# Kernel optimization log

Measured on AMD Instinct MI355X. Metric: run time of the kernel, lower is better.

## Reference

```python
import jax, jax.numpy as jnp
import numpy as np

V_K = 1.0
SIGMA = 0.1
EPS = 1e-10


def setup_inputs() -> dict:
    key = jax.random.key(0)
    ks = jax.random.split(key, 5)
    M, L, N, d, H = 2, 6, 512, 2, 64
    data = jax.random.normal(ks[0], (M, L, N, d), dtype=jnp.float32)
    t_snapshots = jnp.arange(L, dtype=jnp.float32) * 0.1
    w1 = jax.random.normal(ks[1], (H,), dtype=jnp.float32) * 0.5
    b1 = jnp.zeros((H,), jnp.float32)
    W2 = jax.random.normal(ks[2], (H, H), dtype=jnp.float32) / np.float32(np.sqrt(H))
    b2 = jnp.zeros((H,), jnp.float32)
    w3 = jax.random.normal(ks[3], (H,), dtype=jnp.float32) / np.float32(np.sqrt(H))
    b3 = jnp.zeros((), jnp.float32)
    return {"data": data, "t_snapshots": t_snapshots, "w1": w1, "b1": b1,
            "W2": W2, "b2": b2, "w3": w3, "b3": b3}


def _phi(r, w1, b1, W2, b2, w3, b3):
    # scalar-to-scalar tanh MLP applied elementwise to r (any shape)
    h1 = jnp.tanh(r[..., None] * w1 + b1)                      # [..., H]
    h2 = jnp.tanh(jnp.einsum('...h,hk->...k', h1, W2) + b2)    # [..., H]
    return jnp.einsum('...k,k->...', h2, w3) + b3              # [...]


def _loss(data, t, params):
    M, L, N, d = data.shape
    diff = data[:, :, :, None, :] - data[:, :, None, :, :]     # [M,L,N,N,d]
    ssq = jnp.sum(diff * diff, axis=-1)                        # [M,L,N,N]
    dist = jnp.where(ssq > 0, jnp.sqrt(jnp.where(ssq > 0, ssq, 1.0)), 0.0)
    off_diag = ~jnp.eye(N, dtype=bool)                         # [N,N]

    f = lambda r: _phi(r, *params)
    # Phi values on all L snapshots (for energy)
    phi = f(dist)                                              # [M,L,N,N]
    # First/second radial derivatives on current snapshots only (ell = 0..L-2)
    r_cur = dist[:, :-1]                                       # [M,L-1,N,N]
    df = lambda r: jax.jvp(f, (r,), (jnp.ones_like(r),))[1]
    dphi = df(r_cur)                                           # Phi'(r)
    d2phi = jax.jvp(df, (r_cur,), (jnp.ones_like(r_cur),))[1]  # Phi''(r)

    dt = t[1:] - t[:-1]                                        # [L-1]

    # --- drift / dissipation ---
    dist_safe = jnp.maximum(r_cur, EPS)
    unit = diff[:, :-1] / dist_safe[..., None]                 # [M,L-1,N,N,d]
    gphi = jnp.where(off_diag[..., None], dphi[..., None] * unit, 0.0)
    grad_Phi_mean = gphi.sum(axis=3) / N                       # [M,L-1,N,d]
    drift = -V_K * data[:, :-1] - grad_Phi_mean
    total_diss = ((drift ** 2).sum(axis=(2, 3)) / N * dt).sum()

    # --- laplacian / diffusion ---
    lap_phi_mean = jnp.where(off_diag, d2phi, 0.0).sum(axis=-1) / N  # [M,L-1,N]
    lap_sum = V_K * d + lap_phi_mean
    total_diff = (SIGMA ** 2 * lap_sum.mean(axis=-1) * dt).sum()

    # --- energy per snapshot ---
    V_mean = 0.5 * V_K * (data ** 2).sum(axis=-1).mean(axis=-1)      # [M,L]
    Phi_mean = jnp.where(off_diag, phi, 0.0).sum(axis=(-1, -2)) / (N * N)
    E = V_mean + Phi_mean                                            # [M,L]
    total_energy_change = (E[:, 1:] - E[:, :-1]).sum()

    n_pairs = M * (L - 1)
    residual = (total_diss + total_diff - 2.0 * total_energy_change) / n_pairs
    return residual ** 2


def reference(data, t_snapshots, w1, b1, W2, b2, w3, b3):
    return _loss(data, t_snapshots, (w1, b1, W2, b2, w3, b3))
```

## Files before the change

kernel.cpp:

```cpp
#include <hip/hip_runtime.h>
#include <hip/hip_bf16.h>

#define MM 2
#define LL 6
#define NN 512
#define HH 64
#define K_TAB 4096
#define RMAX 16.0f

__device__ __forceinline__ float wave_reduce_sum(float v) {
    #pragma unroll
    for (int m = 32; m > 0; m >>= 1) v += __shfl_xor(v, m, 64);
    return v;
}

__global__ __launch_bounds__(256) void build_table(
        const float* __restrict__ w1, const float* __restrict__ b1,
        const float* __restrict__ W2, const float* __restrict__ b2,
        const float* __restrict__ w3, const float* __restrict__ b3,
        float4* __restrict__ table, float* __restrict__ acc) {
    int gid  = blockIdx.x * blockDim.x + threadIdx.x;
    int wave = gid >> 6;
    int lane = gid & 63;
    if (gid < 64) acc[gid] = 0.0f;
    if (wave >= K_TAB) return;

    float r = (float)wave * (RMAX / (float)K_TAB);

    float w1l = w1[lane];
    float u   = fmaf(r, w1l, b1[lane]);
    float t1  = tanhf(u);
    float e1  = 1.0f - t1 * t1;
    float h1   = t1;
    float h1p  = e1 * w1l;
    float h1pp = -2.0f * t1 * e1 * w1l * w1l;

    float v = b2[lane], vp = 0.0f, vpp = 0.0f;
    #pragma unroll
    for (int h = 0; h < HH; ++h) {
        float a   = __shfl(h1,   h, 64);
        float ap  = __shfl(h1p,  h, 64);
        float app = __shfl(h1pp, h, 64);
        float w   = W2[h * HH + lane];
        v   = fmaf(a,   w, v);
        vp  = fmaf(ap,  w, vp);
        vpp = fmaf(app, w, vpp);
    }
    float t2 = tanhf(v);
    float e2 = 1.0f - t2 * t2;
    float w3l = w3[lane];
    float phik = w3l * t2;
    float dpk  = w3l * e2 * vp;
    float d2k  = w3l * (fmaf(-2.0f * t2 * e2 * vp, vp, e2 * vpp));

    float sphi = wave_reduce_sum(phik);
    float sdp  = wave_reduce_sum(dpk);
    float sd2  = wave_reduce_sum(d2k);
    if (lane == 0)
        table[wave] = make_float4(sphi + b3[0], sdp, sd2, 0.0f);
}

__global__ __launch_bounds__(256) void pair_kernel(
        const float* __restrict__ data, const float4* __restrict__ table,
        float* __restrict__ acc) {
    const int blocks_per_ml = NN / 4;
    int ml = blockIdx.x / blocks_per_ml;
    int i4 = blockIdx.x % blocks_per_ml;

    __shared__ float2 xs[NN];
    __shared__ float  red[4 * 4];

    {
        const float4* src = (const float4*)(data + (size_t)ml * NN * 2);
        ((float4*)xs)[threadIdx.x] = src[threadIdx.x];
    }
    __syncthreads();

    int wv   = threadIdx.x >> 6;
    int lane = threadIdx.x & 63;
    int i    = i4 * 4 + wv;
    float2 xi = xs[i];

    float aphi = 0.0f, ad2 = 0.0f, agx = 0.0f, agy = 0.0f;
    const float scale = (float)K_TAB / RMAX;
    #pragma unroll
    for (int jj = 0; jj < NN / 64; ++jj) {
        int j = jj * 64 + lane;
        if (j == i) continue;
        float2 xj = xs[j];
        float dx = xi.x - xj.x;
        float dy = xi.y - xj.y;
        float ssq = fmaf(dx, dx, dy * dy);
        float rr  = sqrtf(ssq);
        float f   = rr * scale;
        int   idx = (int)f;
        idx = idx > (K_TAB - 2) ? (K_TAB - 2) : idx;
        float frac = f - (float)idx;
        float4 t0 = table[idx];
        float4 t1 = table[idx + 1];
        float phi  = fmaf(frac, t1.x - t0.x, t0.x);
        float dph  = fmaf(frac, t1.y - t0.y, t0.y);
        float d2ph = fmaf(frac, t1.z - t0.z, t0.z);
        float inv_r = 1.0f / fmaxf(rr, 1e-10f);
        aphi += phi;
        ad2  += d2ph;
        float s = dph * inv_r;
        agx = fmaf(s, dx, agx);
        agy = fmaf(s, dy, agy);
    }

    aphi = wave_reduce_sum(aphi);
    ad2  = wave_reduce_sum(ad2);
    agx  = wave_reduce_sum(agx);
    agy  = wave_reduce_sum(agy);

    if (lane == 0) {
        const float invN = 1.0f / (float)NN;
        float driftx = -xi.x - agx * invN;
        float drifty = -xi.y - agy * invN;
        float dr2 = fmaf(driftx, driftx, drifty * drifty);
        float vsq = fmaf(xi.x, xi.x, xi.y * xi.y);
        red[wv * 4 + 0] = aphi;
        red[wv * 4 + 1] = ad2;
        red[wv * 4 + 2] = dr2;
        red[wv * 4 + 3] = vsq;
    }
    __syncthreads();
    if (threadIdx.x < 4) {
        float s = red[0 * 4 + threadIdx.x] + red[1 * 4 + threadIdx.x]
                + red[2 * 4 + threadIdx.x] + red[3 * 4 + threadIdx.x];
        atomicAdd(&acc[ml * 4 + threadIdx.x], s);
    }
}

__global__ void finalize(const float* __restrict__ acc,
                         const float* __restrict__ t,
                         float* __restrict__ out) {
    if (threadIdx.x != 0 || blockIdx.x != 0) return;
    const double N = (double)NN;
    const double SIG2 = 0.01;
    const double VKD  = 2.0;
    double diss = 0.0, diffu = 0.0, dE = 0.0;
    for (int m = 0; m < MM; ++m) {
        double E0 = 0.0;
        for (int l = 0; l < LL; ++l) {
            int ml = m * LL + l;
            double sphi = (double)acc[ml * 4 + 0];
            double sd2  = (double)acc[ml * 4 + 1];
            double sdr  = (double)acc[ml * 4 + 2];
            double sv   = (double)acc[ml * 4 + 3];
            double E = 0.5 * sv / N + sphi / (N * N);
            if (l == 0) E0 = E;
            if (l == LL - 1) dE += E - E0;
            if (l < LL - 1) {
                double dt = (double)t[l + 1] - (double)t[l];
                diss  += sdr / N * dt;
                diffu += SIG2 * (VKD + sd2 / (N * N)) * dt;
            }
        }
    }
    double res = (diss + diffu - 2.0 * dE) / (double)(MM * (LL - 1));
    out[0] = (float)(res * res);
}

extern "C" void kernel_launch(void* const* d_in, const int* in_sizes, int n_in,
                              void* d_out, int out_size, void* d_ws, size_t ws_size,
                              hipStream_t stream) {
    const float* data = (const float*)d_in[0];
    const float* t    = (const float*)d_in[1];
    const float* w1   = (const float*)d_in[2];
    const float* b1   = (const float*)d_in[3];
    const float* W2   = (const float*)d_in[4];
    const float* b2   = (const float*)d_in[5];
    const float* w3   = (const float*)d_in[6];
    const float* b3   = (const float*)d_in[7];

    float4* table = (float4*)d_ws;
    float*  acc   = (float*)((char*)d_ws + (size_t)K_TAB * sizeof(float4));

    build_table<<<(K_TAB * 64) / 256, 256, 0, stream>>>(w1, b1, W2, b2, w3, b3, table, acc);
    pair_kernel<<<MM * LL * (NN / 4), 256, 0, stream>>>(data, table, acc);
    finalize<<<1, 64, 0, stream>>>(acc, t, (float*)d_out);
}
```

Measured before the change: 98.21 us.

## Replace linear lookup table with cubic Hermite spline staged in shared memory

The precomputed table shrinks from 4096 linear-interpolation entries of phi, phi' and phi'' to 1025 Hermite nodes holding phi and phi' only. Phi'' now comes from differentiating the cubic, so the table build drops the second-derivative forward pass. Each pair block builds the cubic coefficients into shared memory and does one LDS read per pair instead of two global gathers. The diagonal skip becomes a select, removing the branch. The trade-offs are lower accuracy for phi'', which is now piecewise linear from a cubic fit, and every one of 1536 blocks rebuilding the 16 KB coefficient table.

```diff
diff --git a/kernel.cpp b/kernel.cpp
--- a/kernel.cpp
+++ b/kernel.cpp
@@ -5,8 +5,11 @@
 #define LL 6
 #define NN 512
 #define HH 64
-#define K_TAB 4096
+#define K_TAB 1024
 #define RMAX 16.0f
+#define H_STEP (RMAX / (float)K_TAB)
+#define HINV   ((float)K_TAB / RMAX)
+
 
 __device__ __forceinline__ float wave_reduce_sum(float v) {
     #pragma unroll
@@ -14,62 +17,67 @@
     return v;
 }
 
-__global__ __launch_bounds__(256) void build_table(
+__global__ __launch_bounds__(256) void build_nodes(
         const float* __restrict__ w1, const float* __restrict__ b1,
         const float* __restrict__ W2, const float* __restrict__ b2,
         const float* __restrict__ w3, const float* __restrict__ b3,
-        float4* __restrict__ table, float* __restrict__ acc) {
+        float2* __restrict__ nodes, float* __restrict__ acc) {
     int gid  = blockIdx.x * blockDim.x + threadIdx.x;
     int wave = gid >> 6;
     int lane = gid & 63;
     if (gid < 64) acc[gid] = 0.0f;
-    if (wave >= K_TAB) return;
+    if (wave > K_TAB) return;
 
-    float r = (float)wave * (RMAX / (float)K_TAB);
+    float r = (float)wave * H_STEP;
 
     float w1l = w1[lane];
     float u   = fmaf(r, w1l, b1[lane]);
     float t1  = tanhf(u);
     float e1  = 1.0f - t1 * t1;
-    float h1   = t1;
-    float h1p  = e1 * w1l;
-    float h1pp = -2.0f * t1 * e1 * w1l * w1l;
+    float h1  = t1;
+    float h1p = e1 * w1l;
 
-    float v = b2[lane], vp = 0.0f, vpp = 0.0f;
+    float v = b2[lane], vp = 0.0f;
     #pragma unroll
     for (int h = 0; h < HH; ++h) {
-        float a   = __shfl(h1,   h, 64);
-        float ap  = __shfl(h1p,  h, 64);
-        float app = __shfl(h1pp, h, 64);
-        float w   = W2[h * HH + lane];
-        v   = fmaf(a,   w, v);
-        vp  = fmaf(ap,  w, vp);
-        vpp = fmaf(app, w, vpp);
+        float a  = __shfl(h1,  h, 64);
+        float ap = __shfl(h1p, h, 64);
+        float w  = W2[h * HH + lane];
+        v  = fmaf(a,  w, v);
+        vp = fmaf(ap, w, vp);
     }
     float t2 = tanhf(v);
     float e2 = 1.0f - t2 * t2;
     float w3l = w3[lane];
     float phik = w3l * t2;
     float dpk  = w3l * e2 * vp;
-    float d2k  = w3l * (fmaf(-2.0f * t2 * e2 * vp, vp, e2 * vpp));
 
     float sphi = wave_reduce_sum(phik);
     float sdp  = wave_reduce_sum(dpk);
-    float sd2  = wave_reduce_sum(d2k);
     if (lane == 0)
-        table[wave] = make_float4(sphi + b3[0], sdp, sd2, 0.0f);
+        nodes[wave] = make_float2(sphi + b3[0], sdp * H_STEP);
 }
 
 __global__ __launch_bounds__(256) void pair_kernel(
-        const float* __restrict__ data, const float4* __restrict__ table,
+        const float* __restrict__ data, const float2* __restrict__ nodes,
         float* __restrict__ acc) {
     const int blocks_per_ml = NN / 4;
     int ml = blockIdx.x / blocks_per_ml;
     int i4 = blockIdx.x % blocks_per_ml;
 
+    __shared__ float4 coef[K_TAB];
     __shared__ float2 xs[NN];
     __shared__ float  red[4 * 4];
 
+    #pragma unroll
+    for (int e = threadIdx.x, it = 0; it < K_TAB / 256; ++it, e += 256) {
+        float2 g0 = nodes[e];
+        float2 g1 = nodes[e + 1];
+        float  d  = g1.x - g0.x;
+        coef[e] = make_float4(g0.x, g0.y,
+                              3.0f * d - 2.0f * g0.y - g1.y,
+                              g0.y + g1.y - 2.0f * d);
+    }
     {
         const float4* src = (const float4*)(data + (size_t)ml * NN * 2);
         ((float4*)xs)[threadIdx.x] = src[threadIdx.x];
@@ -82,28 +90,26 @@
     float2 xi = xs[i];
 
     float aphi = 0.0f, ad2 = 0.0f, agx = 0.0f, agy = 0.0f;
-    const float scale = (float)K_TAB / RMAX;
     #pragma unroll
     for (int jj = 0; jj < NN / 64; ++jj) {
         int j = jj * 64 + lane;
-        if (j == i) continue;
         float2 xj = xs[j];
         float dx = xi.x - xj.x;
         float dy = xi.y - xj.y;
         float ssq = fmaf(dx, dx, dy * dy);
         float rr  = sqrtf(ssq);
-        float f   = rr * scale;
+        float f   = rr * HINV;
         int   idx = (int)f;
-        idx = idx > (K_TAB - 2) ? (K_TAB - 2) : idx;
-        float frac = f - (float)idx;
-        float4 t0 = table[idx];
-        float4 t1 = table[idx + 1];
-        float phi  = fmaf(frac, t1.x - t0.x, t0.x);
-        float dph  = fmaf(frac, t1.y - t0.y, t0.y);
-        float d2ph = fmaf(frac, t1.z - t0.z, t0.z);
+        idx = idx > (K_TAB - 1) ? (K_TAB - 1) : idx;
+        float t = f - (float)idx;
+        float4 c = coef[idx];
+        float phi  = fmaf(t, fmaf(t, fmaf(t, c.w, c.z), c.y), c.x);
+        float dph  = fmaf(t, fmaf(t, 3.0f * c.w, 2.0f * c.z), c.y) * HINV;
+        float d2ph = fmaf(t, 6.0f * c.w, 2.0f * c.z) * (HINV * HINV);
         float inv_r = 1.0f / fmaxf(rr, 1e-10f);
-        aphi += phi;
-        ad2  += d2ph;
+        bool off = (j != i);
+        aphi += off ? phi  : 0.0f;
+        ad2  += off ? d2ph : 0.0f;
         float s = dph * inv_r;
         agx = fmaf(s, dx, agx);
         agy = fmaf(s, dy, agy);
@@ -175,10 +181,10 @@
     const float* w3   = (const float*)d_in[6];
     const float* b3   = (const float*)d_in[7];
 
-    float4* table = (float4*)d_ws;
-    float*  acc   = (float*)((char*)d_ws + (size_t)K_TAB * sizeof(float4));
+    float2* nodes = (float2*)d_ws;
+    float*  acc   = (float*)((char*)d_ws + 16384);
 
-    build_table<<<(K_TAB * 64) / 256, 256, 0, stream>>>(w1, b1, W2, b2, w3, b3, table, acc);
-    pair_kernel<<<MM * LL * (NN / 4), 256, 0, stream>>>(data, table, acc);
+    build_nodes<<<257, 256, 0, stream>>>(w1, b1, W2, b2, w3, b3, nodes, acc);
+    pair_kernel<<<MM * LL * (NN / 4), 256, 0, stream>>>(data, nodes, acc);
     finalize<<<1, 64, 0, stream>>>(acc, t, (float*)d_out);
 }
```

Result: faster. 87.38 us (-11.0%).
